# Kernel optimization log

Hardware: AMD Instinct MI355X
Metric: run time of the kernel (lower is better)

## Reference

```python
import jax, jax.numpy as jnp
import numpy as np

D_MODEL = 1024
NHEAD = 16
D_K = D_MODEL // NHEAD


def setup_inputs() -> dict:
    key = jax.random.key(0)
    ks = jax.random.split(key, 11)
    B, S = 2, 2048
    scale = 1.0 / np.sqrt(D_MODEL)
    inp = {
        "q": jax.random.normal(ks[0], (B, S, D_MODEL), jnp.float32),
        "k": jax.random.normal(ks[1], (B, S, D_MODEL), jnp.float32),
        "v": jax.random.normal(ks[2], (B, S, D_MODEL), jnp.float32),
        "Wq": jax.random.normal(ks[3], (D_MODEL, D_MODEL), jnp.float32) * scale,
        "bq": jnp.zeros((D_MODEL,), jnp.float32),
        "Wk": jax.random.normal(ks[4], (D_MODEL, D_MODEL), jnp.float32) * scale,
        "bk": jnp.zeros((D_MODEL,), jnp.float32),
        "Wv": jax.random.normal(ks[5], (D_MODEL, D_MODEL), jnp.float32) * scale,
        "bv": jnp.zeros((D_MODEL,), jnp.float32),
        "Wo": jax.random.normal(ks[6], (D_MODEL, D_MODEL), jnp.float32) * scale,
        "bo": jnp.zeros((D_MODEL,), jnp.float32),
    }
    return inp


def reference(q, k, v, Wq, bq, Wk, bk, Wv, bv, Wo, bo):
    B, S, _ = q.shape
    # Linear projections (torch Linear: x @ W.T + b), split into heads
    def proj(x, W, b):
        y = jnp.einsum('bsd,ed->bse', x, W) + b
        return y.reshape(B, -1, NHEAD, D_K).transpose(0, 2, 1, 3)  # [B,H,S,Dk]

    qh = proj(q, Wq, bq)
    kh = proj(k, Wk, bk)
    vh = proj(v, Wv, bv)

    scores = jnp.einsum('bhqd,bhkd->bhqk', qh, kh) / jnp.sqrt(
        jnp.asarray(D_K, qh.dtype))
    attn = jax.nn.softmax(scores, axis=-1)  # dropout is identity in eval
    out = jnp.einsum('bhqk,bhkd->bhqd', attn, vh)
    out = out.transpose(0, 2, 1, 3).reshape(B, S, D_MODEL)
    return jnp.einsum('bsd,ed->bse', out, Wo) + bo
```

## Files before the change

### kernel.cpp

```cpp
#include <hip/hip_runtime.h>
#include <stdint.h>
#include <stddef.h>

#define D_MODEL 1024
#define NHEAD   16
#define DK      64
#define BB      2
#define SS      2048
#define NTOK    (BB*SS)

#define SCALE_Q 0.18033688011f

typedef short  short8 __attribute__((ext_vector_type(8)));
typedef __bf16 bf16x8 __attribute__((ext_vector_type(8)));
typedef float  f32x4  __attribute__((ext_vector_type(4)));

__device__ __forceinline__ unsigned short f2bf(float x){
  unsigned int u = __builtin_bit_cast(unsigned int, x);
  u += 0x7fffu + ((u >> 16) & 1u);
  return (unsigned short)(u >> 16);
}

__device__ __forceinline__ unsigned int pack_bf2(float x, float y){
  unsigned int a = __builtin_bit_cast(unsigned int, x) + 0x8000u;
  unsigned int b = __builtin_bit_cast(unsigned int, y) + 0x8000u;
  return __builtin_amdgcn_perm(b, a, 0x07060302u);
}

__device__ __forceinline__ unsigned int cvt_pk_bf16(float lo, float hi){
  unsigned int r;
  asm("v_cvt_pk_bf16_f32 %0, %1, %2" : "=v"(r) : "v"(lo), "v"(hi));
  return r;
}

__device__ __forceinline__ float fast_exp2(float x){
#if __has_builtin(__builtin_amdgcn_exp2f)
  return __builtin_amdgcn_exp2f(x);
#else
  return exp2f(x);
#endif
}

__device__ __forceinline__ f32x4 mfma16(bf16x8 a, bf16x8 b, f32x4 c){
  return __builtin_amdgcn_mfma_f32_16x16x32_bf16(a, b, c, 0, 0, 0);
}

__device__ __forceinline__ void async16(const void* g, void* lds){
  __builtin_amdgcn_global_load_lds(
      (const __attribute__((address_space(1))) unsigned int*)g,
      (__attribute__((address_space(3))) unsigned int*)lds,
      16, 0, 0);
}

__global__ __launch_bounds__(256) void cast_bf16_all(
    const float* __restrict__ q,  const float* __restrict__ k,  const float* __restrict__ v,
    const float* __restrict__ wq, const float* __restrict__ wk, const float* __restrict__ wv,
    const float* __restrict__ wo,
    unsigned short* __restrict__ qb,  unsigned short* __restrict__ kb,  unsigned short* __restrict__ vb,
    unsigned short* __restrict__ wqb, unsigned short* __restrict__ wkb, unsigned short* __restrict__ wvb,
    unsigned short* __restrict__ wob)
{
  const float* src; unsigned short* dst; int n;
  switch (blockIdx.y){
    case 0: src = q;  dst = qb;  n = NTOK*D_MODEL;    break;
    case 1: src = k;  dst = kb;  n = NTOK*D_MODEL;    break;
    case 2: src = v;  dst = vb;  n = NTOK*D_MODEL;    break;
    case 3: src = wq; dst = wqb; n = D_MODEL*D_MODEL; break;
    case 4: src = wk; dst = wkb; n = D_MODEL*D_MODEL; break;
    case 5: src = wv; dst = wvb; n = D_MODEL*D_MODEL; break;
    default: src = wo; dst = wob; n = D_MODEL*D_MODEL; break;
  }
  int i = (blockIdx.x * 256 + threadIdx.x) * 8;
  if (i >= n) return;
  float4 a = *(const float4*)(src + i);
  float4 b = *(const float4*)(src + i + 4);
  short8 o;
  o[0] = (short)f2bf(a.x); o[1] = (short)f2bf(a.y);
  o[2] = (short)f2bf(a.z); o[3] = (short)f2bf(a.w);
  o[4] = (short)f2bf(b.x); o[5] = (short)f2bf(b.y);
  o[6] = (short)f2bf(b.z); o[7] = (short)f2bf(b.w);
  *(short8*)(dst + i) = o;
}

__global__ __launch_bounds__(256) void qkv_gemm(
    const unsigned short* __restrict__ qb, const unsigned short* __restrict__ kb,
    const unsigned short* __restrict__ vb,
    const unsigned short* __restrict__ wqb, const unsigned short* __restrict__ wkb,
    const unsigned short* __restrict__ wvb,
    const float* __restrict__ bq, const float* __restrict__ bk, const float* __restrict__ bv,
    unsigned short* __restrict__ Qh, unsigned short* __restrict__ Kh, unsigned short* __restrict__ Vt)
{
  __shared__ __align__(16) unsigned short S[128*192];

  int bid = blockIdx.x;
  const int id = (bid & 7) * 96 + (bid >> 3);
  const int z = id >> 8, r = id & 255;
  const unsigned short *A, *Bt; const float* bias; unsigned short* C;
  int bm, bn, N, brow; float scale;
  if (z == 0){ A = qb;  Bt = wqb; bias = bq; C = Qh; bm = (r>>3)*128; bn = (r&7)*128; N = 1024; brow = 0; scale = SCALE_Q; }
  else if (z == 1){ A = kb;  Bt = wkb; bias = bk; C = Kh; bm = (r>>3)*128; bn = (r&7)*128; N = 1024; brow = 0; scale = 1.0f; }
  else            { A = wvb; Bt = vb;  bias = bv; C = Vt; bm = (r&7)*128; bn = (r>>3)*128; N = 4096; brow = 1; scale = 1.0f; }
  const int K = 1024;
  const int tid  = threadIdx.x, lane = tid & 63, w = tid >> 6;
  const int quad = lane >> 4,   l16  = lane & 15;
  const int wm = w >> 1, wn = w & 1;
  const int fsl = (quad ^ ((l16 >> 2) & 3)) << 3;

  const unsigned short* asrc[2];
  const unsigned short* bsrc[2];
  #pragma unroll
  for (int c = 0; c < 2; ++c){
    int s = (w*2 + c)*64 + lane;
    int row = s >> 2, c4 = s & 3;
    int cs = (c4 ^ ((row >> 2) & 3)) << 3;
    asrc[c] = A  + (size_t)(bm + row)*K + cs;
    bsrc[c] = Bt + (size_t)(bn + row)*K + cs;
  }

  unsigned short *rdA = S,             *rdB = S + 4096;
  unsigned short *nxA = S + 8192,      *nxB = S + 12288;
  unsigned short *stA = S + 16384,     *stB = S + 20480;

  #pragma unroll
  for (int c = 0; c < 2; ++c){
    async16(asrc[c], (char*)rdA + (w*2 + c)*1024);
    async16(bsrc[c], (char*)rdB + (w*2 + c)*1024);
    asrc[c] += 32; bsrc[c] += 32;
  }
  #pragma unroll
  for (int c = 0; c < 2; ++c){
    async16(asrc[c], (char*)nxA + (w*2 + c)*1024);
    async16(bsrc[c], (char*)nxB + (w*2 + c)*1024);
    asrc[c] += 32; bsrc[c] += 32;
  }

  f32x4 acc[4][4] = {};
  for (int t = 0; t < 32; ++t){
    #pragma unroll
    for (int c = 0; c < 2; ++c){
      async16(asrc[c], (char*)stA + (w*2 + c)*1024);
      async16(bsrc[c], (char*)stB + (w*2 + c)*1024);
      asrc[c] += 32; bsrc[c] += 32;
    }
    asm volatile("s_waitcnt vmcnt(8)\n\ts_barrier" ::: "memory");

    bf16x8 af[4], bf[4];
    #pragma unroll
    for (int mt = 0; mt < 4; ++mt){
      af[mt] = *(const bf16x8*)&rdA[(wm*64 + mt*16 + l16)*32 + fsl];
      bf[mt] = *(const bf16x8*)&rdB[(wn*64 + mt*16 + l16)*32 + fsl];
    }
    #pragma unroll
    for (int mt = 0; mt < 4; ++mt)
      #pragma unroll
      for (int nt = 0; nt < 4; ++nt)
        acc[mt][nt] = mfma16(bf[nt], af[mt], acc[mt][nt]);

    asm volatile("s_waitcnt lgkmcnt(0)\n\ts_barrier" ::: "memory");
    unsigned short* tA = rdA; rdA = nxA; nxA = stA; stA = tA;
    unsigned short* tB = rdB; rdB = nxB; nxB = stB; stB = tB;
  }
  asm volatile("s_waitcnt vmcnt(0)\n\ts_barrier" ::: "memory");

  #pragma unroll
  for (int nt = 0; nt < 4; ++nt){
    int nl = wn*64 + nt*16 + 4*quad;
    float4 b4;
    if (!brow) b4 = *(const float4*)&bias[bn + nl];
    #pragma unroll
    for (int mt = 0; mt < 4; ++mt){
      int ml = wm*64 + mt*16 + l16;
      float bmv = brow ? bias[bm + ml] : 0.0f;
      float v0 = (acc[mt][nt][0] + (brow ? bmv : b4.x)) * scale;
      float v1 = (acc[mt][nt][1] + (brow ? bmv : b4.y)) * scale;
      float v2 = (acc[mt][nt][2] + (brow ? bmv : b4.z)) * scale;
      float v3 = (acc[mt][nt][3] + (brow ? bmv : b4.w)) * scale;
      uint2 p; p.x = pack_bf2(v0, v1); p.y = pack_bf2(v2, v3);
      int gl = nl >> 2;
      if (brow){
        int g3 = gl & 7;
        gl = (gl & ~7) | ((g3 & 3)*2 + (g3 >> 2));
      }
      int gs = gl ^ (ml & 14);
      *(uint2*)&S[ml*128 + gs*4] = p;
    }
  }
  __syncthreads();
  {
    int rr_ = tid >> 1, hf = tid & 1;
    size_t rowbase = (size_t)(bm + rr_) * N + bn;
    #pragma unroll
    for (int i = 0; i < 8; ++i){
      int gg = hf*16 + i*2;
      uint4 d = *(const uint4*)&S[rr_*128 + ((gg ^ (rr_ & 14)) << 2)];
      *(uint4*)&C[rowbase + gg*4] = d;
    }
  }
}

__global__ __launch_bounds__(256) void gemm_out(
    const unsigned short* __restrict__ A, const unsigned short* __restrict__ Bt,
    const float* __restrict__ bias, float* __restrict__ C)
{
  __shared__ __align__(16) unsigned short As[2][64*64];
  __shared__ __align__(16) unsigned short Bs[2][128*64];
  const int K = 1024, N = 1024;
  const int tid  = threadIdx.x, lane = tid & 63, w = tid >> 6;
  const int quad = lane >> 4,   l16  = lane & 15;
  int bid = blockIdx.x;
  const int id = (bid & 7) * 64 + (bid >> 3);
  const int bm = (id >> 3) * 64, bn = (id & 7) * 128;
  const int sw = l16 & 7;

  const unsigned short* asrc[2];
  const unsigned short* bsrc[4];
  #pragma unroll
  for (int c = 0; c < 2; ++c){
    int chunk = (w*2 + c)*64 + lane;
    int row = chunk >> 3, c8 = chunk & 7;
    asrc[c] = A + (size_t)(bm + row)*K + ((c8 ^ (row & 7)) << 3);
  }
  #pragma unroll
  for (int c = 0; c < 4; ++c){
    int chunk = (w*4 + c)*64 + lane;
    int row = chunk >> 3, c8 = chunk & 7;
    bsrc[c] = Bt + (size_t)(bn + row)*K + ((c8 ^ (row & 7)) << 3);
  }

  #pragma unroll
  for (int c = 0; c < 2; ++c){ async16(asrc[c], (char*)As[0] + (w*2 + c)*1024); asrc[c] += 64; }
  #pragma unroll
  for (int c = 0; c < 4; ++c){ async16(bsrc[c], (char*)Bs[0] + (w*4 + c)*1024); bsrc[c] += 64; }

  f32x4 acc[4][2] = {};
  for (int t = 0; t < 16; ++t){
    const int cur = t & 1;
    #pragma unroll
    for (int c = 0; c < 2; ++c){
      async16(asrc[c], (char*)As[1 - cur] + (w*2 + c)*1024); asrc[c] += 64;
    }
    #pragma unroll
    for (int c = 0; c < 4; ++c){
      async16(bsrc[c], (char*)Bs[1 - cur] + (w*4 + c)*1024); bsrc[c] += 64;
    }
    asm volatile("s_waitcnt vmcnt(6)\n\ts_barrier" ::: "memory");

    const unsigned short* Ac = As[cur];
    bf16x8 af[4][2], bf[2][2];
    #pragma unroll
    for (int mt = 0; mt < 4; ++mt)
      #pragma unroll
      for (int ks = 0; ks < 2; ++ks)
        af[mt][ks] = *(const bf16x8*)&Ac[(mt*16 + l16)*64 + (((ks*4 + quad) ^ sw) << 3)];
    #pragma unroll
    for (int nt = 0; nt < 2; ++nt)
      #pragma unroll
      for (int ks = 0; ks < 2; ++ks)
        bf[nt][ks] = *(const bf16x8*)&Bs[cur][(w*32 + nt*16 + l16)*64 + (((ks*4 + quad) ^ sw) << 3)];
    #pragma unroll
    for (int ks = 0; ks < 2; ++ks)
      #pragma unroll
      for (int mt = 0; mt < 4; ++mt)
        #pragma unroll
        for (int nt = 0; nt < 2; ++nt)
          acc[mt][nt] = mfma16(af[mt][ks], bf[nt][ks], acc[mt][nt]);

    asm volatile("s_waitcnt lgkmcnt(0)\n\ts_barrier" ::: "memory");
  }

  #pragma unroll
  for (int mt = 0; mt < 4; ++mt){
    #pragma unroll
    for (int nt = 0; nt < 2; ++nt){
      int col = bn + w*32 + nt*16 + l16;
      float bc = bias[col];
      #pragma unroll
      for (int rr = 0; rr < 4; ++rr){
        int row = bm + mt*16 + quad*4 + rr;
        C[(size_t)row*N + col] = acc[mt][nt][rr] + bc;
      }
    }
  }
}

__global__ __launch_bounds__(512, 4) void attn(
    const unsigned short* __restrict__ Qh, const unsigned short* __restrict__ Kh,
    const unsigned short* __restrict__ Vt, unsigned short* __restrict__ ctx)
{
  __shared__ __align__(16) unsigned short Kbuf[2][64*64];
  __shared__ __align__(16) unsigned short Vbuf[2][64*64];
  __shared__ __align__(16) unsigned short QP[128*64];

  const int tid  = threadIdx.x, lane = tid & 63, w = tid >> 6;
  const int quad = lane >> 4,   l16  = lane & 15;
  const int b = blockIdx.y >> 4, h = blockIdx.y & 15;
  const int q0 = blockIdx.x * 128;
  const int sw = l16 & 7;

  #pragma unroll
  for (int c = 0; c < 2; ++c){
    int s = (w*2 + c)*64 + lane;
    int row = s >> 3, c8 = s & 7;
    async16(Qh + (size_t)(b*SS + q0 + row)*D_MODEL + h*DK + ((c8 ^ (row & 7)) << 3),
            (char*)QP + (w*2 + c)*1024);
  }

  const unsigned short* ksrc;
  const unsigned short* vsrc;
  {
    const unsigned short* Kpp = Kh + (size_t)(b*SS)*D_MODEL + h*DK;
    const unsigned short* Vpp = Vt + (size_t)(h*DK)*NTOK + b*SS;
    int s = w*64 + lane;
    int row = s >> 3, c8 = s & 7;
    int cs = (c8 ^ (row & 7)) << 3;
    ksrc = Kpp + (size_t)row*D_MODEL + cs;
    vsrc = Vpp + (size_t)row*NTOK  + cs;
  }

  async16(ksrc, (char*)Kbuf[0] + w*1024);
  async16(vsrc, (char*)Vbuf[0] + w*1024);
  ksrc += 64*D_MODEL;
  vsrc += 64;
  __syncthreads();

  bf16x8 bq[2];
  #pragma unroll
  for (int ks = 0; ks < 2; ++ks)
    bq[ks] = *(const bf16x8*)&QP[(w*16 + l16)*64 + (((ks*4 + quad) ^ sw) << 3)];

  f32x4 acc[4] = {};
  float l0a = 0.0f, l0b = 0.0f;

  for (int it = 0; it < 32; ++it){
    const int cur = it & 1;
    async16(ksrc, (char*)Kbuf[1 - cur] + w*1024);
    async16(vsrc, (char*)Vbuf[1 - cur] + w*1024);
    ksrc += 64*D_MODEL;
    vsrc += 64;
    asm volatile("s_waitcnt vmcnt(2)\n\ts_barrier" ::: "memory");

    const unsigned short* Kc = Kbuf[cur];
    const unsigned short* Vc = Vbuf[cur];

    bf16x8 kf[4][2];
    #pragma unroll
    for (int mt = 0; mt < 4; ++mt)
      #pragma unroll
      for (int ks = 0; ks < 2; ++ks)
        kf[mt][ks] = *(const bf16x8*)&Kc[(mt*16 + l16)*64 + (((ks*4 + quad) ^ sw) << 3)];

    bf16x8 vf[4][2];
    #pragma unroll
    for (int nt = 0; nt < 4; ++nt)
      #pragma unroll
      for (int ks = 0; ks < 2; ++ks)
        vf[nt][ks] = *(const bf16x8*)&Vc[(nt*16 + l16)*64 + (((ks*4 + quad) ^ sw) << 3)];

    f32x4 s0[4] = {};
    #pragma unroll
    for (int mt = 0; mt < 4; ++mt)
      #pragma unroll
      for (int ks = 0; ks < 2; ++ks)
        s0[mt] = mfma16(kf[mt][ks], bq[ks], s0[mt]);

    float sa = 0.0f, sb = 0.0f;
    #pragma unroll
    for (int mt = 0; mt < 4; ++mt)
      #pragma unroll
      for (int rr = 0; rr < 4; ++rr){
        float p0 = fast_exp2(s0[mt][rr]); s0[mt][rr] = p0;
        if (mt & 1) sb += p0; else sa += p0;
      }
    l0a += sa; l0b += sb;

    bf16x8 bp[2];
    #pragma unroll
    for (int ks = 0; ks < 2; ++ks){
      uint4 t;
      t.x = cvt_pk_bf16(s0[2*ks  ][0], s0[2*ks  ][1]);
      t.y = cvt_pk_bf16(s0[2*ks  ][2], s0[2*ks  ][3]);
      t.z = cvt_pk_bf16(s0[2*ks+1][0], s0[2*ks+1][1]);
      t.w = cvt_pk_bf16(s0[2*ks+1][2], s0[2*ks+1][3]);
      bp[ks] = __builtin_bit_cast(bf16x8, t);
    }

    #pragma unroll
    for (int nt = 0; nt < 4; ++nt)
      #pragma unroll
      for (int ks = 0; ks < 2; ++ks)
        acc[nt] = mfma16(vf[nt][ks], bp[ks], acc[nt]);

    asm volatile("s_waitcnt lgkmcnt(0)\n\ts_barrier" ::: "memory");
  }

  float t = l0a + l0b;
  t += __shfl_xor(t, 16);
  t += __shfl_xor(t, 32);
  const float inv = 1.0f / t;

  {
    const int pr = (w*16 + l16)*64;
    #pragma unroll
    for (int nt = 0; nt < 4; ++nt){
      int c8  = nt*2 + (quad >> 1);
      int off = ((c8 ^ sw) << 3) + (quad & 1)*4;
      uint2 p;
      p.x = pack_bf2(acc[nt][0]*inv, acc[nt][1]*inv);
      p.y = pack_bf2(acc[nt][2]*inv, acc[nt][3]*inv);
      *(uint2*)&QP[pr + off] = p;
    }
  }
  asm volatile("s_waitcnt lgkmcnt(0)" ::: "memory");
  {
    int r  = w*16 + (lane >> 2);
    int j0 = lane & 3;
    unsigned short* dst = ctx + (size_t)(b*SS + q0 + r)*D_MODEL + h*DK;
    #pragma unroll
    for (int i = 0; i < 2; ++i){
      int j = j0 + i*4;
      uint4 d = *(const uint4*)&QP[r*64 + ((j ^ (r & 7)) << 3)];
      *(uint4*)(dst + j*8) = d;
    }
  }
}

extern "C" void kernel_launch(void* const* d_in, const int* in_sizes, int n_in,
                              void* d_out, int out_size, void* d_ws, size_t ws_size,
                              hipStream_t stream) {
  const float* q  = (const float*)d_in[0];
  const float* k  = (const float*)d_in[1];
  const float* v  = (const float*)d_in[2];
  const float* Wq = (const float*)d_in[3];
  const float* bq = (const float*)d_in[4];
  const float* Wk = (const float*)d_in[5];
  const float* bk = (const float*)d_in[6];
  const float* Wv = (const float*)d_in[7];
  const float* bv = (const float*)d_in[8];
  const float* Wo = (const float*)d_in[9];
  const float* bo = (const float*)d_in[10];

  char* ws = (char*)d_ws;
  const size_t TOKB = (size_t)NTOK * D_MODEL * 2;
  const size_t WB   = (size_t)D_MODEL * D_MODEL * 2;
  unsigned short* qb  = (unsigned short*)ws;             ws += TOKB;
  unsigned short* kb  = (unsigned short*)ws;             ws += TOKB;
  unsigned short* vb  = (unsigned short*)ws;             ws += TOKB;
  unsigned short* wqb = (unsigned short*)ws;             ws += WB;
  unsigned short* wkb = (unsigned short*)ws;             ws += WB;
  unsigned short* wvb = (unsigned short*)ws;             ws += WB;
  unsigned short* wob = (unsigned short*)ws;             ws += WB;
  unsigned short* Qh  = (unsigned short*)ws;             ws += TOKB;
  unsigned short* Kh  = (unsigned short*)ws;             ws += TOKB;
  unsigned short* Vt  = (unsigned short*)ws;             ws += TOKB;
  unsigned short* ctx = (unsigned short*)ws;             ws += TOKB;
  ws += 4096;

  cast_bf16_all<<<dim3(2048, 7), 256, 0, stream>>>(q, k, v, Wq, Wk, Wv, Wo,
                                                   qb, kb, vb, wqb, wkb, wvb, wob);
  qkv_gemm<<<dim3(768), 256, 0, stream>>>(qb, kb, vb, wqb, wkb, wvb,
                                          bq, bk, bv, Qh, Kh, Vt);
  attn<<<dim3(SS/128, BB*NHEAD), 512, 0, stream>>>(Qh, Kh, Vt, ctx);
  gemm_out<<<dim3(512), 256, 0, stream>>>(ctx, wob, bo, (float*)d_out);
}
```

Measured before the change: 216.4 us.

## Double-buffer GEMM fragments in registers and drop per-step LDS barrier

Unrolls the projection GEMM main loop by two and keeps two sets of bf16 fragment registers. The LDS reads for the next k-tile are issued right after the MFMAs on the current tile, and the wait-then-barrier moves after the MFMAs. This removes the separate lgkmcnt(0)+barrier step each iteration and overlaps LDS reads with matrix math. In exchange it raises register pressure and depends on subtle ordering of the triple-buffered LDS slots to stay race-free.

```diff
diff --git a/kernel.cpp b/kernel.cpp
--- a/kernel.cpp
+++ b/kernel.cpp
@@ -117,9 +117,9 @@
     bsrc[c] = Bt + (size_t)(bn + row)*K + cs;
   }
 
-  unsigned short *rdA = S,             *rdB = S + 4096;
-  unsigned short *nxA = S + 8192,      *nxB = S + 12288;
-  unsigned short *stA = S + 16384,     *stB = S + 20480;
+  unsigned short *rdA = S,         *rdB = S + 4096;
+  unsigned short *nxA = S + 8192,  *nxB = S + 12288;
+  unsigned short *stA = S + 16384, *stB = S + 20480;
 
   #pragma unroll
   for (int c = 0; c < 2; ++c){
@@ -133,32 +133,56 @@
     async16(bsrc[c], (char*)nxB + (w*2 + c)*1024);
     asrc[c] += 32; bsrc[c] += 32;
   }
+  asm volatile("s_waitcnt vmcnt(4)\n\ts_barrier" ::: "memory");
+
+  bf16x8 afA[4], bfA[4], afB[4], bfB[4];
+  #pragma unroll
+  for (int mt = 0; mt < 4; ++mt){
+    afA[mt] = *(const bf16x8*)&rdA[(wm*64 + mt*16 + l16)*32 + fsl];
+    bfA[mt] = *(const bf16x8*)&rdB[(wn*64 + mt*16 + l16)*32 + fsl];
+  }
 
   f32x4 acc[4][4] = {};
-  for (int t = 0; t < 32; ++t){
+  for (int t = 0; t < 32; t += 2){
     #pragma unroll
     for (int c = 0; c < 2; ++c){
       async16(asrc[c], (char*)stA + (w*2 + c)*1024);
       async16(bsrc[c], (char*)stB + (w*2 + c)*1024);
       asrc[c] += 32; bsrc[c] += 32;
     }
-    asm volatile("s_waitcnt vmcnt(8)\n\ts_barrier" ::: "memory");
-
-    bf16x8 af[4], bf[4];
+    #pragma unroll
+    for (int mt = 0; mt < 4; ++mt)
+      #pragma unroll
+      for (int nt = 0; nt < 4; ++nt)
+        acc[mt][nt] = mfma16(bfA[nt], afA[mt], acc[mt][nt]);
+    asm volatile("s_waitcnt vmcnt(4)\n\ts_barrier" ::: "memory");
     #pragma unroll
     for (int mt = 0; mt < 4; ++mt){
-      af[mt] = *(const bf16x8*)&rdA[(wm*64 + mt*16 + l16)*32 + fsl];
-      bf[mt] = *(const bf16x8*)&rdB[(wn*64 + mt*16 + l16)*32 + fsl];
+      afB[mt] = *(const bf16x8*)&nxA[(wm*64 + mt*16 + l16)*32 + fsl];
+      bfB[mt] = *(const bf16x8*)&nxB[(wn*64 + mt*16 + l16)*32 + fsl];
+    }
+    { unsigned short* tA = rdA; rdA = nxA; nxA = stA; stA = tA;
+      unsigned short* tB = rdB; rdB = nxB; nxB = stB; stB = tB; }
+
+    #pragma unroll
+    for (int c = 0; c < 2; ++c){
+      async16(asrc[c], (char*)stA + (w*2 + c)*1024);
+      async16(bsrc[c], (char*)stB + (w*2 + c)*1024);
+      asrc[c] += 32; bsrc[c] += 32;
     }
     #pragma unroll
     for (int mt = 0; mt < 4; ++mt)
       #pragma unroll
       for (int nt = 0; nt < 4; ++nt)
-        acc[mt][nt] = mfma16(bf[nt], af[mt], acc[mt][nt]);
-
-    asm volatile("s_waitcnt lgkmcnt(0)\n\ts_barrier" ::: "memory");
-    unsigned short* tA = rdA; rdA = nxA; nxA = stA; stA = tA;
-    unsigned short* tB = rdB; rdB = nxB; nxB = stB; stB = tB;
+        acc[mt][nt] = mfma16(bfB[nt], afB[mt], acc[mt][nt]);
+    asm volatile("s_waitcnt vmcnt(4)\n\ts_barrier" ::: "memory");
+    #pragma unroll
+    for (int mt = 0; mt < 4; ++mt){
+      afA[mt] = *(const bf16x8*)&nxA[(wm*64 + mt*16 + l16)*32 + fsl];
+      bfA[mt] = *(const bf16x8*)&nxB[(wn*64 + mt*16 + l16)*32 + fsl];
+    }
+    { unsigned short* tA = rdA; rdA = nxA; nxA = stA; stA = tA;
+      unsigned short* tB = rdB; rdB = nxB; nxB = stB; stB = tB; }
   }
   asm volatile("s_waitcnt vmcnt(0)\n\ts_barrier" ::: "memory");
 
```

Measured after the change: 216.0 us. No clear change (-0.2%).

## Fuse fp32-to-bf16 cast into QKV GEMM operand loads, drop separate cast kernel

Applied to the files above, without the earlier changes.

Removes the standalone cast kernel. The QKV GEMM now reads fp32 activations and weights directly, converts them to bf16 in registers and writes them to LDS through a two-stage register-prefetch double buffer. The async global-to-LDS triple buffering is gone. Extra blocks appended to the QKV launch cast Wo for the output GEMM. This avoids writing and re-reading bf16 copies of q/k/v and the weights, at the cost of twice the global read bytes per tile, conversion ALU work inside the main loop, and a simpler pipeline with less latency hiding.

```diff
diff --git a/kernel.cpp b/kernel.cpp
--- a/kernel.cpp
+++ b/kernel.cpp
@@ -11,15 +11,8 @@
 
 #define SCALE_Q 0.18033688011f
 
-typedef short  short8 __attribute__((ext_vector_type(8)));
 typedef __bf16 bf16x8 __attribute__((ext_vector_type(8)));
 typedef float  f32x4  __attribute__((ext_vector_type(4)));
-
-__device__ __forceinline__ unsigned short f2bf(float x){
-  unsigned int u = __builtin_bit_cast(unsigned int, x);
-  u += 0x7fffu + ((u >> 16) & 1u);
-  return (unsigned short)(u >> 16);
-}
 
 __device__ __forceinline__ unsigned int pack_bf2(float x, float y){
   unsigned int a = __builtin_bit_cast(unsigned int, x) + 0x8000u;
@@ -52,97 +45,90 @@
       16, 0, 0);
 }
 
-__global__ __launch_bounds__(256) void cast_bf16_all(
+__global__ __launch_bounds__(256) void qkv_gemm(
     const float* __restrict__ q,  const float* __restrict__ k,  const float* __restrict__ v,
-    const float* __restrict__ wq, const float* __restrict__ wk, const float* __restrict__ wv,
-    const float* __restrict__ wo,
-    unsigned short* __restrict__ qb,  unsigned short* __restrict__ kb,  unsigned short* __restrict__ vb,
-    unsigned short* __restrict__ wqb, unsigned short* __restrict__ wkb, unsigned short* __restrict__ wvb,
-    unsigned short* __restrict__ wob)
+    const float* __restrict__ Wq, const float* __restrict__ Wk, const float* __restrict__ Wv,
+    const float* __restrict__ Wo,
+    const float* __restrict__ bq, const float* __restrict__ bk, const float* __restrict__ bv,
+    unsigned short* __restrict__ Qh, unsigned short* __restrict__ Kh,
+    unsigned short* __restrict__ Vt, unsigned short* __restrict__ wob)
 {
-  const float* src; unsigned short* dst; int n;
-  switch (blockIdx.y){
-    case 0: src = q;  dst = qb;  n = NTOK*D_MODEL;    break;
-    case 1: src = k;  dst = kb;  n = NTOK*D_MODEL;    break;
-    case 2: src = v;  dst = vb;  n = NTOK*D_MODEL;    break;
-    case 3: src = wq; dst = wqb; n = D_MODEL*D_MODEL; break;
-    case 4: src = wk; dst = wkb; n = D_MODEL*D_MODEL; break;
-    case 5: src = wv; dst = wvb; n = D_MODEL*D_MODEL; break;
-    default: src = wo; dst = wob; n = D_MODEL*D_MODEL; break;
-  }
-  int i = (blockIdx.x * 256 + threadIdx.x) * 8;
-  if (i >= n) return;
-  float4 a = *(const float4*)(src + i);
-  float4 b = *(const float4*)(src + i + 4);
-  short8 o;
-  o[0] = (short)f2bf(a.x); o[1] = (short)f2bf(a.y);
-  o[2] = (short)f2bf(a.z); o[3] = (short)f2bf(a.w);
-  o[4] = (short)f2bf(b.x); o[5] = (short)f2bf(b.y);
-  o[6] = (short)f2bf(b.z); o[7] = (short)f2bf(b.w);
-  *(short8*)(dst + i) = o;
-}
-
-__global__ __launch_bounds__(256) void qkv_gemm(
-    const unsigned short* __restrict__ qb, const unsigned short* __restrict__ kb,
-    const unsigned short* __restrict__ vb,
-    const unsigned short* __restrict__ wqb, const unsigned short* __restrict__ wkb,
-    const unsigned short* __restrict__ wvb,
-    const float* __restrict__ bq, const float* __restrict__ bk, const float* __restrict__ bv,
-    unsigned short* __restrict__ Qh, unsigned short* __restrict__ Kh, unsigned short* __restrict__ Vt)
-{
-  __shared__ __align__(16) unsigned short S[128*192];
-
-  int bid = blockIdx.x;
+  const int bid = blockIdx.x;
+  if (bid >= 768){
+    int ibase = (bid - 768)*(256*32) + threadIdx.x*8;
+    #pragma unroll
+    for (int c = 0; c < 4; ++c){
+      int i = ibase + c*2048;
+      float4 a = *(const float4*)(Wo + i);
+      float4 b = *(const float4*)(Wo + i + 4);
+      uint4 o;
+      o.x = cvt_pk_bf16(a.x, a.y); o.y = cvt_pk_bf16(a.z, a.w);
+      o.z = cvt_pk_bf16(b.x, b.y); o.w = cvt_pk_bf16(b.z, b.w);
+      *(uint4*)(wob + i) = o;
+    }
+    return;
+  }
+
+  __shared__ __align__(16) unsigned short S[128*128];
   const int id = (bid & 7) * 96 + (bid >> 3);
   const int z = id >> 8, r = id & 255;
-  const unsigned short *A, *Bt; const float* bias; unsigned short* C;
+  const float *A, *Bt; const float* bias; unsigned short* C;
   int bm, bn, N, brow; float scale;
-  if (z == 0){ A = qb;  Bt = wqb; bias = bq; C = Qh; bm = (r>>3)*128; bn = (r&7)*128; N = 1024; brow = 0; scale = SCALE_Q; }
-  else if (z == 1){ A = kb;  Bt = wkb; bias = bk; C = Kh; bm = (r>>3)*128; bn = (r&7)*128; N = 1024; brow = 0; scale = 1.0f; }
-  else            { A = wvb; Bt = vb;  bias = bv; C = Vt; bm = (r&7)*128; bn = (r>>3)*128; N = 4096; brow = 1; scale = 1.0f; }
+  if (z == 0){ A = q;  Bt = Wq; bias = bq; C = Qh; bm = (r>>3)*128; bn = (r&7)*128; N = 1024; brow = 0; scale = SCALE_Q; }
+  else if (z == 1){ A = k;  Bt = Wk; bias = bk; C = Kh; bm = (r>>3)*128; bn = (r&7)*128; N = 1024; brow = 0; scale = 1.0f; }
+  else            { A = Wv; Bt = v;  bias = bv; C = Vt; bm = (r&7)*128; bn = (r>>3)*128; N = 4096; brow = 1; scale = 1.0f; }
   const int K = 1024;
   const int tid  = threadIdx.x, lane = tid & 63, w = tid >> 6;
   const int quad = lane >> 4,   l16  = lane & 15;
   const int wm = w >> 1, wn = w & 1;
   const int fsl = (quad ^ ((l16 >> 2) & 3)) << 3;
 
-  const unsigned short* asrc[2];
-  const unsigned short* bsrc[2];
+  const float* asrc[2];
+  const float* bsrc[2];
+  int dsto[2];
   #pragma unroll
   for (int c = 0; c < 2; ++c){
     int s = (w*2 + c)*64 + lane;
     int row = s >> 2, c4 = s & 3;
-    int cs = (c4 ^ ((row >> 2) & 3)) << 3;
-    asrc[c] = A  + (size_t)(bm + row)*K + cs;
-    bsrc[c] = Bt + (size_t)(bn + row)*K + cs;
-  }
-
-  unsigned short *rdA = S,             *rdB = S + 4096;
-  unsigned short *nxA = S + 8192,      *nxB = S + 12288;
-  unsigned short *stA = S + 16384,     *stB = S + 20480;
-
-  #pragma unroll
-  for (int c = 0; c < 2; ++c){
-    async16(asrc[c], (char*)rdA + (w*2 + c)*1024);
-    async16(bsrc[c], (char*)rdB + (w*2 + c)*1024);
-    asrc[c] += 32; bsrc[c] += 32;
-  }
-  #pragma unroll
-  for (int c = 0; c < 2; ++c){
-    async16(asrc[c], (char*)nxA + (w*2 + c)*1024);
-    async16(bsrc[c], (char*)nxB + (w*2 + c)*1024);
-    asrc[c] += 32; bsrc[c] += 32;
-  }
+    int col = (c4 ^ ((row >> 2) & 3)) << 3;
+    asrc[c] = A  + (size_t)(bm + row)*K + col;
+    bsrc[c] = Bt + (size_t)(bn + row)*K + col;
+    dsto[c] = (w*2 + c)*1024 + lane*16;
+  }
+
+  unsigned short *rdA = S,         *rdB = S + 4096;
+  unsigned short *wrA = S + 8192,  *wrB = S + 12288;
+
+  {
+    #pragma unroll
+    for (int c = 0; c < 2; ++c){
+      float4 a0 = *(const float4*)asrc[c];
+      float4 a1 = *(const float4*)(asrc[c] + 4);
+      float4 b0 = *(const float4*)bsrc[c];
+      float4 b1 = *(const float4*)(bsrc[c] + 4);
+      asrc[c] += 32; bsrc[c] += 32;
+      uint4 pa, pb;
+      pa.x = cvt_pk_bf16(a0.x, a0.y); pa.y = cvt_pk_bf16(a0.z, a0.w);
+      pa.z = cvt_pk_bf16(a1.x, a1.y); pa.w = cvt_pk_bf16(a1.z, a1.w);
+      pb.x = cvt_pk_bf16(b0.x, b0.y); pb.y = cvt_pk_bf16(b0.z, b0.w);
+      pb.z = cvt_pk_bf16(b1.x, b1.y); pb.w = cvt_pk_bf16(b1.z, b1.w);
+      *(uint4*)((char*)rdA + dsto[c]) = pa;
+      *(uint4*)((char*)rdB + dsto[c]) = pb;
+    }
+  }
+  __syncthreads();
 
   f32x4 acc[4][4] = {};
-  for (int t = 0; t < 32; ++t){
-    #pragma unroll
-    for (int c = 0; c < 2; ++c){
-      async16(asrc[c], (char*)stA + (w*2 + c)*1024);
-      async16(bsrc[c], (char*)stB + (w*2 + c)*1024);
-      asrc[c] += 32; bsrc[c] += 32;
-    }
-    asm volatile("s_waitcnt vmcnt(8)\n\ts_barrier" ::: "memory");
+  for (int t = 0; t < 31; ++t){
+    float4 a00 = *(const float4*)asrc[0];
+    float4 a01 = *(const float4*)(asrc[0] + 4);
+    float4 a10 = *(const float4*)asrc[1];
+    float4 a11 = *(const float4*)(asrc[1] + 4);
+    float4 b00 = *(const float4*)bsrc[0];
+    float4 b01 = *(const float4*)(bsrc[0] + 4);
+    float4 b10 = *(const float4*)bsrc[1];
+    float4 b11 = *(const float4*)(bsrc[1] + 4);
+    asrc[0] += 32; asrc[1] += 32; bsrc[0] += 32; bsrc[1] += 32;
 
     bf16x8 af[4], bf[4];
     #pragma unroll
@@ -156,11 +142,38 @@
       for (int nt = 0; nt < 4; ++nt)
         acc[mt][nt] = mfma16(bf[nt], af[mt], acc[mt][nt]);
 
-    asm volatile("s_waitcnt lgkmcnt(0)\n\ts_barrier" ::: "memory");
-    unsigned short* tA = rdA; rdA = nxA; nxA = stA; stA = tA;
-    unsigned short* tB = rdB; rdB = nxB; nxB = stB; stB = tB;
-  }
-  asm volatile("s_waitcnt vmcnt(0)\n\ts_barrier" ::: "memory");
+    uint4 p;
+    p.x = cvt_pk_bf16(a00.x, a00.y); p.y = cvt_pk_bf16(a00.z, a00.w);
+    p.z = cvt_pk_bf16(a01.x, a01.y); p.w = cvt_pk_bf16(a01.z, a01.w);
+    *(uint4*)((char*)wrA + dsto[0]) = p;
+    p.x = cvt_pk_bf16(a10.x, a10.y); p.y = cvt_pk_bf16(a10.z, a10.w);
+    p.z = cvt_pk_bf16(a11.x, a11.y); p.w = cvt_pk_bf16(a11.z, a11.w);
+    *(uint4*)((char*)wrA + dsto[1]) = p;
+    p.x = cvt_pk_bf16(b00.x, b00.y); p.y = cvt_pk_bf16(b00.z, b00.w);
+    p.z = cvt_pk_bf16(b01.x, b01.y); p.w = cvt_pk_bf16(b01.z, b01.w);
+    *(uint4*)((char*)wrB + dsto[0]) = p;
+    p.x = cvt_pk_bf16(b10.x, b10.y); p.y = cvt_pk_bf16(b10.z, b10.w);
+    p.z = cvt_pk_bf16(b11.x, b11.y); p.w = cvt_pk_bf16(b11.z, b11.w);
+    *(uint4*)((char*)wrB + dsto[1]) = p;
+
+    __syncthreads();
+    unsigned short* tA = rdA; rdA = wrA; wrA = tA;
+    unsigned short* tB = rdB; rdB = wrB; wrB = tB;
+  }
+  {
+    bf16x8 af[4], bf[4];
+    #pragma unroll
+    for (int mt = 0; mt < 4; ++mt){
+      af[mt] = *(const bf16x8*)&rdA[(wm*64 + mt*16 + l16)*32 + fsl];
+      bf[mt] = *(const bf16x8*)&rdB[(wn*64 + mt*16 + l16)*32 + fsl];
+    }
+    #pragma unroll
+    for (int mt = 0; mt < 4; ++mt)
+      #pragma unroll
+      for (int nt = 0; nt < 4; ++nt)
+        acc[mt][nt] = mfma16(bf[nt], af[mt], acc[mt][nt]);
+  }
+  __syncthreads();
 
   #pragma unroll
   for (int nt = 0; nt < 4; ++nt){
@@ -175,14 +188,14 @@
       float v1 = (acc[mt][nt][1] + (brow ? bmv : b4.y)) * scale;
       float v2 = (acc[mt][nt][2] + (brow ? bmv : b4.z)) * scale;
       float v3 = (acc[mt][nt][3] + (brow ? bmv : b4.w)) * scale;
-      uint2 p; p.x = pack_bf2(v0, v1); p.y = pack_bf2(v2, v3);
+      uint2 p2; p2.x = pack_bf2(v0, v1); p2.y = pack_bf2(v2, v3);
       int gl = nl >> 2;
       if (brow){
         int g3 = gl & 7;
         gl = (gl & ~7) | ((g3 & 3)*2 + (g3 >> 2));
       }
       int gs = gl ^ (ml & 14);
-      *(uint2*)&S[ml*128 + gs*4] = p;
+      *(uint2*)&S[ml*128 + gs*4] = p2;
     }
   }
   __syncthreads();
@@ -442,12 +455,6 @@
   char* ws = (char*)d_ws;
   const size_t TOKB = (size_t)NTOK * D_MODEL * 2;
   const size_t WB   = (size_t)D_MODEL * D_MODEL * 2;
-  unsigned short* qb  = (unsigned short*)ws;             ws += TOKB;
-  unsigned short* kb  = (unsigned short*)ws;             ws += TOKB;
-  unsigned short* vb  = (unsigned short*)ws;             ws += TOKB;
-  unsigned short* wqb = (unsigned short*)ws;             ws += WB;
-  unsigned short* wkb = (unsigned short*)ws;             ws += WB;
-  unsigned short* wvb = (unsigned short*)ws;             ws += WB;
   unsigned short* wob = (unsigned short*)ws;             ws += WB;
   unsigned short* Qh  = (unsigned short*)ws;             ws += TOKB;
   unsigned short* Kh  = (unsigned short*)ws;             ws += TOKB;
@@ -455,10 +462,8 @@
   unsigned short* ctx = (unsigned short*)ws;             ws += TOKB;
   ws += 4096;
 
-  cast_bf16_all<<<dim3(2048, 7), 256, 0, stream>>>(q, k, v, Wq, Wk, Wv, Wo,
-                                                   qb, kb, vb, wqb, wkb, wvb, wob);
-  qkv_gemm<<<dim3(768), 256, 0, stream>>>(qb, kb, vb, wqb, wkb, wvb,
-                                          bq, bk, bv, Qh, Kh, Vt);
+  qkv_gemm<<<dim3(896), 256, 0, stream>>>(q, k, v, Wq, Wk, Wv, Wo,
+                                          bq, bk, bv, Qh, Kh, Vt, wob);
   attn<<<dim3(SS/128, BB*NHEAD), 512, 0, stream>>>(Qh, Kh, Vt, ctx);
   gemm_out<<<dim3(512), 256, 0, stream>>>(ctx, wob, bo, (float*)d_out);
 }
```

Measured after the change: 241.8 us. 1.12x slower.
